# Kernel optimization log

Measured on AMD Instinct MI355X. Metric: run time of the kernel, lower is better.

## Reference

```python
import jax, jax.numpy as jnp
import numpy as np

N = 1_000_000
E = 32_000_000

def setup_inputs() -> dict:
    key = jax.random.key(0)
    k = jax.random.split(key, 7)
    x = jax.random.normal(k[0], (N, 1), dtype=jnp.float32)
    edge_index = jax.random.randint(k[1], (2, E), 0, N, dtype=jnp.int64)
    # lin1: 1 -> 4
    W1 = jax.random.normal(k[2], (4, 1), dtype=jnp.float32) * 0.5
    b1 = jax.random.normal(k[3], (4,), dtype=jnp.float32) * 0.1
    # lin2: 4 -> 1
    W2 = jax.random.normal(k[4], (1, 4), dtype=jnp.float32) * 0.5
    b2 = jax.random.normal(k[5], (1,), dtype=jnp.float32) * 0.1
    # SAGEConv lin_l: 1 -> 1, no bias, no root weight
    Wsage = jax.random.normal(k[6], (1, 1), dtype=jnp.float32) * 0.5
    return {"x": x, "edge_index": edge_index, "W1": W1, "b1": b1,
            "W2": W2, "b2": b2, "Wsage": Wsage}

def reference(x, edge_index, W1, b1, W2, b2, Wsage):
    # tiny MLP: 1 -> 4 -> 1
    h = jax.nn.relu(x @ W1.T + b1)          # [N,4]
    h = h @ W2.T + b2                        # [N,1]
    # SAGEConv mean aggregation: edges flow src -> dst
    src, dst = edge_index[0], edge_index[1]
    n = x.shape[0]
    agg = jax.ops.segment_sum(h[src], dst, num_segments=n)          # [N,1]
    cnt = jax.ops.segment_sum(jnp.ones((src.shape[0], 1), h.dtype), dst,
                              num_segments=n)                        # [N,1]
    mean = agg / jnp.maximum(cnt, 1.0)       # isolated nodes -> 0 (PyG behavior)
    return mean @ Wsage.T                    # lin_l, no root weight, no bias
```

## Files before the change

kernel.cpp:

```cpp
#include <hip/hip_runtime.h>
#include <hip/hip_fp16.h>


#define NBINS    256
#define BSHIFT   12
#define DMASK    4095
#define NBLK     1024
#define STHREADS 512
#define EPT      16
#define TILE     (STHREADS * EPT)
#define PACK_SCALE 1048576.0

__global__ void detect_dtype_kernel(const int* __restrict__ ei, int* __restrict__ flag) {
    if (threadIdx.x == 0 && blockIdx.x == 0) {
        int is64 = 1;
        for (int i = 1; i < 256; i += 2) {
            if (ei[i] != 0) { is64 = 0; break; }
        }
        *flag = is64;
    }
}

__global__ void node_kernel(const float* __restrict__ x,
                            const float* __restrict__ W1,
                            const float* __restrict__ b1,
                            const float* __restrict__ W2,
                            const float* __restrict__ b2,
                            unsigned short* __restrict__ h2f16,
                            int n) {
    int i = blockIdx.x * blockDim.x + threadIdx.x;
    if (i >= n) return;
    float xi = x[i];
    float acc = b2[0];
#pragma unroll
    for (int j = 0; j < 4; ++j) {
        float t = fmaxf(W1[j] * xi + b1[j], 0.0f);
        acc += W2[j] * t;
    }
    h2f16[i] = __half_as_ushort(__float2half(acc));
}

__global__ void __launch_bounds__(STHREADS)
scatter_tile_kernel(const int* __restrict__ ei,
                    const unsigned short* __restrict__ h2f16,
                    unsigned int* __restrict__ entries,
                    int* __restrict__ index,
                    const int* __restrict__ flag,
                    long long E, long long chunk, int tpb, int ntiles) {
    __shared__ unsigned int ents[TILE];
    __shared__ int hist[NBINS];
    __shared__ int toff[NBINS];
    __shared__ int s_total;

    const int t = threadIdx.x;
    long long start = (long long)blockIdx.x * chunk;
    long long end   = start + chunk; if (end > E) end = E;
    const int is64 = *flag;
    const long long* e64 = (const long long*)ei;

    int ti = 0;
    for (long long tbase = start; tbase < end; tbase += TILE, ++ti) {
        for (int i = t; i < NBINS; i += STHREADS) hist[i] = 0;
        __syncthreads();

        int sk[EPT], dk[EPT];
        if (is64) {
#pragma unroll
            for (int k = 0; k < EPT; ++k) {
                long long e = tbase + (long long)k * STHREADS + t;
                if (e < end) {
                    sk[k] = (int)__builtin_nontemporal_load(&e64[e]);
                    dk[k] = (int)__builtin_nontemporal_load(&e64[E + e]);
                } else { sk[k] = 0; dk[k] = -1; }
            }
        } else {
#pragma unroll
            for (int k = 0; k < EPT; ++k) {
                long long e = tbase + (long long)k * STHREADS + t;
                if (e < end) {
                    sk[k] = __builtin_nontemporal_load(&ei[e]);
                    dk[k] = __builtin_nontemporal_load(&ei[E + e]);
                } else { sk[k] = 0; dk[k] = -1; }
            }
        }

        unsigned int hv[EPT];
#pragma unroll
        for (int k = 0; k < EPT; ++k) hv[k] = (unsigned int)h2f16[sk[k]];

        int rk[EPT];
#pragma unroll
        for (int k = 0; k < EPT; ++k)
            if (dk[k] >= 0) rk[k] = atomicAdd(&hist[dk[k] >> BSHIFT], 1);
        __syncthreads();

        if (t < 64) {
            const int base = t * 4;
            int a0 = hist[base], a1 = hist[base + 1],
                a2 = hist[base + 2], a3 = hist[base + 3];
            int s  = a0 + a1 + a2 + a3;
            int sc = s;
#pragma unroll
            for (int off = 1; off < 64; off <<= 1) {
                int up = __shfl_up(sc, off, 64);
                if (t >= off) sc += up;
            }
            int excl = sc - s;
            toff[base]     = excl;
            toff[base + 1] = excl + a0;
            toff[base + 2] = excl + a0 + a1;
            toff[base + 3] = excl + a0 + a1 + a2;
            if (t == 63) s_total = sc;
        }
        __syncthreads();

#pragma unroll
        for (int k = 0; k < EPT; ++k) {
            if (dk[k] >= 0) {
                int slot = toff[dk[k] >> BSHIFT] + rk[k];
                ents[slot] = ((unsigned int)(dk[k] & DMASK) << 16) | hv[k];
            }
        }
        __syncthreads();

        const int tilecount = s_total;
        const int g = blockIdx.x * tpb + ti;
        unsigned int* gout = entries + (long long)g * TILE;
        for (int j = t; j < tilecount; j += STHREADS)
            __builtin_nontemporal_store(ents[j], &gout[j]);
        if (t < NBINS)
            __builtin_nontemporal_store(toff[t], &index[(long long)t * ntiles + g]);
        else if (t == NBINS)
            __builtin_nontemporal_store(tilecount, &index[(long long)NBINS * ntiles + g]);
        __syncthreads();
    }
}

__global__ void __launch_bounds__(1024, 8)
aggregate_kernel(const unsigned int* __restrict__ entries,
                 const int* __restrict__ index,
                 double* __restrict__ partial,
                 int ntiles) {
    __shared__ double acc[4096];
    const int b   = blockIdx.x >> 1;
    const int sub = blockIdx.x & 1;
    const int t   = threadIdx.x;
    for (int i = t; i < 4096; i += blockDim.x) acc[i] = 0.0;
    __syncthreads();

    const int half_t = ntiles >> 1;
    const int gbase  = sub * half_t;
    const int wave = t >> 6;
    const int lane = t & 63;
    const int half = lane >> 5;
    const int hl   = lane & 31;
    const int* __restrict__ rowS = index + (long long)b * ntiles;
    const int* __restrict__ rowE = index + (long long)(b + 1) * ntiles;

    for (int g = gbase + wave * 2 + half; g < gbase + half_t; g += 32) {
        int s = rowS[g];
        int e = rowE[g];
        const unsigned int* run = entries + (long long)g * TILE;
        for (int i = s + hl; i < e; i += 32) {
            unsigned int ent = __builtin_nontemporal_load(&run[i]);
            int dlow = (int)(ent >> 16);
            float v  = __half2float(__ushort_as_half((unsigned short)(ent & 0xFFFFu)));
            atomicAdd(&acc[dlow], (double)v + PACK_SCALE);
        }
    }
    __syncthreads();

    double* p = partial + (long long)blockIdx.x * 4096;
    for (int i = t; i < 4096; i += blockDim.x)
        __builtin_nontemporal_store(acc[i], &p[i]);
}

__global__ void finalize_kernel(const double* __restrict__ partial,
                                const float* __restrict__ Wsage,
                                float* __restrict__ out,
                                int n) {
    int i = blockIdx.x * blockDim.x + threadIdx.x;
    if (i >= n) return;
    int b    = i >> BSHIFT;
    int dlow = i & DMASK;
    double v = partial[(long long)(b * 2) * 4096 + dlow]
             + partial[(long long)(b * 2 + 1) * 4096 + dlow];
    double cnt = nearbyint(v * (1.0 / PACK_SCALE));
    double agg = v - cnt * PACK_SCALE;
    out[i] = (float)(agg / fmax(cnt, 1.0)) * Wsage[0];
}


__global__ void node_f32_kernel(const float* __restrict__ x,
                                const float* __restrict__ W1,
                                const float* __restrict__ b1,
                                const float* __restrict__ W2,
                                const float* __restrict__ b2,
                                float* __restrict__ h2,
                                int n) {
    int i = blockIdx.x * blockDim.x + threadIdx.x;
    if (i >= n) return;
    float xi = x[i];
    float acc = b2[0];
#pragma unroll
    for (int j = 0; j < 4; ++j) {
        float t = fmaxf(W1[j] * xi + b1[j], 0.0f);
        acc += W2[j] * t;
    }
    h2[i] = acc;
}

__global__ void zero_packed_kernel(double* __restrict__ packed, int n) {
    int i = blockIdx.x * blockDim.x + threadIdx.x;
    if (i < n) packed[i] = 0.0;
}

__global__ void edge_atomic_kernel(const int* __restrict__ ei,
                                   const float* __restrict__ h2,
                                   double* __restrict__ packed,
                                   const int* __restrict__ flag,
                                   long long E) {
    long long i      = (long long)blockIdx.x * blockDim.x + threadIdx.x;
    long long stride = (long long)gridDim.x * blockDim.x;
    const int is64 = *flag;
    if (is64) {
        const long long* e64 = (const long long*)ei;
        for (long long e = i; e < E; e += stride) {
            int s = (int)e64[e];
            int d = (int)e64[E + e];
            atomicAdd(&packed[d], (double)h2[s] + PACK_SCALE);
        }
    } else {
        for (long long e = i; e < E; e += stride) {
            int s = ei[e];
            int d = ei[E + e];
            atomicAdd(&packed[d], (double)h2[s] + PACK_SCALE);
        }
    }
}

__global__ void out_packed_kernel(const double* __restrict__ packed,
                                  const float* __restrict__ Wsage,
                                  float* __restrict__ out,
                                  int n) {
    int i = blockIdx.x * blockDim.x + threadIdx.x;
    if (i >= n) return;
    double v   = packed[i];
    double cnt = nearbyint(v * (1.0 / PACK_SCALE));
    double agg = v - cnt * PACK_SCALE;
    out[i] = (float)(agg / fmax(cnt, 1.0)) * Wsage[0];
}

extern "C" void kernel_launch(void* const* d_in, const int* in_sizes, int n_in,
                              void* d_out, int out_size, void* d_ws, size_t ws_size,
                              hipStream_t stream) {
    const float* x     = (const float*)d_in[0];
    const int*   ei    = (const int*)d_in[1];
    const float* W1    = (const float*)d_in[2];
    const float* b1    = (const float*)d_in[3];
    const float* W2    = (const float*)d_in[4];
    const float* b2    = (const float*)d_in[5];
    const float* Wsage = (const float*)d_in[6];

    const int       n = in_sizes[0];
    const long long E = (long long)in_sizes[1] / 2;

    const long long chunk  = (E + NBLK - 1) / NBLK;
    const int       tpb    = (int)((chunk + TILE - 1) / TILE);
    const int       ntiles = NBLK * tpb;

    const size_t entries_b = (size_t)ntiles * TILE * 4;
    const size_t index_b   = (size_t)(NBINS + 1) * ntiles * 4;
    const size_t partial_b = (size_t)2 * NBINS * 4096 * 8;
    const size_t h2_b      = (size_t)n * 2;
    const size_t need      = entries_b + index_b + partial_b + h2_b + 64;

    if (ws_size >= need) {
        unsigned int*   entries = (unsigned int*)d_ws;
        int*            index   = (int*)((char*)d_ws + entries_b);
        double*         partial = (double*)((char*)d_ws + entries_b + index_b);
        unsigned short* h2f16   = (unsigned short*)((char*)d_ws + entries_b + index_b + partial_b);
        int*            flag    = (int*)((char*)d_ws + entries_b + index_b + partial_b + h2_b);

        detect_dtype_kernel<<<1, 64, 0, stream>>>(ei, flag);
        {
            int threads = 256;
            int blocks  = (n + threads - 1) / threads;
            node_kernel<<<blocks, threads, 0, stream>>>(x, W1, b1, W2, b2, h2f16, n);
        }
        scatter_tile_kernel<<<NBLK, STHREADS, 0, stream>>>(ei, h2f16, entries, index,
                                                           flag, E, chunk, tpb, ntiles);
        aggregate_kernel<<<NBINS * 2, 1024, 0, stream>>>(entries, index, partial, ntiles);
        {
            int threads = 256;
            int blocks  = (n + threads - 1) / threads;
            finalize_kernel<<<blocks, threads, 0, stream>>>(partial, Wsage,
                                                            (float*)d_out, n);
        }
    } else {
        double* packed = (double*)d_ws;
        float*  h2     = (float*)d_out;
        int*    flag   = (int*)(packed + n);

        detect_dtype_kernel<<<1, 64, 0, stream>>>(ei, flag);
        {
            int threads = 256;
            int blocks  = (n + threads - 1) / threads;
            node_f32_kernel<<<blocks, threads, 0, stream>>>(x, W1, b1, W2, b2, h2, n);
            zero_packed_kernel<<<blocks, threads, 0, stream>>>(packed, n);
        }
        edge_atomic_kernel<<<4096, 256, 0, stream>>>(ei, h2, packed, flag, E);
        {
            int threads = 256;
            int blocks  = (n + threads - 1) / threads;
            out_packed_kernel<<<blocks, threads, 0, stream>>>(packed, Wsage,
                                                              (float*)d_out, n);
        }
    }
}
```

Measured before the change: 310.8 us.

## Move h gather from scatter pass into aggregate pass and pack source index

The scatter kernel no longer gathers the fp16 node value per edge. It packs the 12-bit local destination with a 20-bit source index, and the aggregate kernel gathers h2f16[src] when it consumes each entry. The aggregate grid changes to 4 sub-blocks per bin with 512 threads, and the tile write-out uses 16-byte vector stores instead of nontemporal scalar stores. The aim is to take the dependent random gather off the scatter critical path and raise parallelism in aggregation. In exchange, the random gather now sits inside the atomic loop, and the fast path is limited to n up to 2^20.

```diff
diff --git a/kernel.cpp b/kernel.cpp
--- a/kernel.cpp
+++ b/kernel.cpp
@@ -5,10 +5,12 @@
 #define NBINS    256
 #define BSHIFT   12
 #define DMASK    4095
+#define SRCBITS  20
 #define NBLK     1024
 #define STHREADS 512
 #define EPT      16
 #define TILE     (STHREADS * EPT)
+#define NSUB     4
 #define PACK_SCALE 1048576.0
 
 __global__ void detect_dtype_kernel(const int* __restrict__ ei, int* __restrict__ flag) {
@@ -42,7 +44,6 @@
 
 __global__ void __launch_bounds__(STHREADS)
 scatter_tile_kernel(const int* __restrict__ ei,
-                    const unsigned short* __restrict__ h2f16,
                     unsigned int* __restrict__ entries,
                     int* __restrict__ index,
                     const int* __restrict__ flag,
@@ -83,10 +84,6 @@
                 } else { sk[k] = 0; dk[k] = -1; }
             }
         }
-
-        unsigned int hv[EPT];
-#pragma unroll
-        for (int k = 0; k < EPT; ++k) hv[k] = (unsigned int)h2f16[sk[k]];
 
         int rk[EPT];
 #pragma unroll
@@ -118,7 +115,8 @@
         for (int k = 0; k < EPT; ++k) {
             if (dk[k] >= 0) {
                 int slot = toff[dk[k] >> BSHIFT] + rk[k];
-                ents[slot] = ((unsigned int)(dk[k] & DMASK) << 16) | hv[k];
+                ents[slot] = ((unsigned int)(dk[k] & DMASK) << SRCBITS)
+                           | (unsigned int)sk[k];
             }
         }
         __syncthreads();
@@ -126,8 +124,11 @@
         const int tilecount = s_total;
         const int g = blockIdx.x * tpb + ti;
         unsigned int* gout = entries + (long long)g * TILE;
-        for (int j = t; j < tilecount; j += STHREADS)
-            __builtin_nontemporal_store(ents[j], &gout[j]);
+        const int tc4 = (tilecount + 3) & ~3;
+        for (int j = t * 4; j < tc4; j += STHREADS * 4) {
+            uint4 val = *(const uint4*)&ents[j];
+            *(uint4*)&gout[j] = val;
+        }
         if (t < NBINS)
             __builtin_nontemporal_store(toff[t], &index[(long long)t * ntiles + g]);
         else if (t == NBINS)
@@ -136,35 +137,35 @@
     }
 }
 
-__global__ void __launch_bounds__(1024, 8)
+__global__ void __launch_bounds__(512)
 aggregate_kernel(const unsigned int* __restrict__ entries,
                  const int* __restrict__ index,
+                 const unsigned short* __restrict__ h2f16,
                  double* __restrict__ partial,
                  int ntiles) {
     __shared__ double acc[4096];
-    const int b   = blockIdx.x >> 1;
-    const int sub = blockIdx.x & 1;
+    const int b   = blockIdx.x >> 2;
+    const int sub = blockIdx.x & 3;
     const int t   = threadIdx.x;
     for (int i = t; i < 4096; i += blockDim.x) acc[i] = 0.0;
     __syncthreads();
 
-    const int half_t = ntiles >> 1;
-    const int gbase  = sub * half_t;
-    const int wave = t >> 6;
-    const int lane = t & 63;
-    const int half = lane >> 5;
-    const int hl   = lane & 31;
+    const int quarter = ntiles >> 2;
+    const int gbase   = sub * quarter;
+    const int grp = t >> 5;
+    const int hl  = t & 31;
     const int* __restrict__ rowS = index + (long long)b * ntiles;
     const int* __restrict__ rowE = index + (long long)(b + 1) * ntiles;
 
-    for (int g = gbase + wave * 2 + half; g < gbase + half_t; g += 32) {
+    for (int g = gbase + grp; g < gbase + quarter; g += 16) {
         int s = rowS[g];
         int e = rowE[g];
         const unsigned int* run = entries + (long long)g * TILE;
         for (int i = s + hl; i < e; i += 32) {
             unsigned int ent = __builtin_nontemporal_load(&run[i]);
-            int dlow = (int)(ent >> 16);
-            float v  = __half2float(__ushort_as_half((unsigned short)(ent & 0xFFFFu)));
+            int dlow = (int)(ent >> SRCBITS);
+            int src  = (int)(ent & ((1u << SRCBITS) - 1));
+            float v  = __half2float(__ushort_as_half(h2f16[src]));
             atomicAdd(&acc[dlow], (double)v + PACK_SCALE);
         }
     }
@@ -183,8 +184,8 @@
     if (i >= n) return;
     int b    = i >> BSHIFT;
     int dlow = i & DMASK;
-    double v = partial[(long long)(b * 2) * 4096 + dlow]
-             + partial[(long long)(b * 2 + 1) * 4096 + dlow];
+    const double* p = partial + (long long)(b * NSUB) * 4096 + dlow;
+    double v = p[0] + p[4096] + p[2 * 4096] + p[3 * 4096];
     double cnt = nearbyint(v * (1.0 / PACK_SCALE));
     double agg = v - cnt * PACK_SCALE;
     out[i] = (float)(agg / fmax(cnt, 1.0)) * Wsage[0];
@@ -271,11 +272,11 @@
 
     const size_t entries_b = (size_t)ntiles * TILE * 4;
     const size_t index_b   = (size_t)(NBINS + 1) * ntiles * 4;
-    const size_t partial_b = (size_t)2 * NBINS * 4096 * 8;
+    const size_t partial_b = (size_t)NSUB * NBINS * 4096 * 8;
     const size_t h2_b      = (size_t)n * 2;
     const size_t need      = entries_b + index_b + partial_b + h2_b + 64;
 
-    if (ws_size >= need) {
+    if (ws_size >= need && n <= (1 << SRCBITS)) {
         unsigned int*   entries = (unsigned int*)d_ws;
         int*            index   = (int*)((char*)d_ws + entries_b);
         double*         partial = (double*)((char*)d_ws + entries_b + index_b);
@@ -288,9 +289,10 @@
             int blocks  = (n + threads - 1) / threads;
             node_kernel<<<blocks, threads, 0, stream>>>(x, W1, b1, W2, b2, h2f16, n);
         }
-        scatter_tile_kernel<<<NBLK, STHREADS, 0, stream>>>(ei, h2f16, entries, index,
+        scatter_tile_kernel<<<NBLK, STHREADS, 0, stream>>>(ei, entries, index,
                                                            flag, E, chunk, tpb, ntiles);
-        aggregate_kernel<<<NBINS * 2, 1024, 0, stream>>>(entries, index, partial, ntiles);
+        aggregate_kernel<<<NBINS * NSUB, 512, 0, stream>>>(entries, index, h2f16,
+                                                           partial, ntiles);
         {
             int threads = 256;
             int blocks  = (n + threads - 1) / threads;
```

Result: slower. 337.7 us (+8.7%).
